# Kernel optimization log

Measured on AMD Instinct MI355X. Metric: run time of the kernel, lower is better.

The kernel has to match this reference:

```python
import jax, jax.numpy as jnp
import numpy as np

# Dims
B, L = 64, 64            # bs*n_vars, patch_num
C, K = 32, 100           # cluster_num, top-k tokens per cluster
D_MODEL, H, D_LLM = 128, 8, 768
D_KEYS = D_MODEL // H    # 16
TEMP = 1.0 / np.sqrt(D_KEYS)
SCALE = 0.02             # param init scale for numerical stability


def setup_inputs() -> dict:
    key = jax.random.key(0)
    ks = jax.random.split(key, 8)
    return {
        "topk_token_embeddings": jax.random.normal(ks[0], (C, K, D_LLM), jnp.float32),
        "ts_emb": jax.random.normal(ks[1], (B, L, D_MODEL), jnp.float32),
        "cluster_probs": jax.random.uniform(ks[2], (B, L, C), jnp.float32),
        # per-cluster projections; last input column is a fused bias (+1 dim)
        "Wq": jax.random.normal(ks[3], (C, H * D_KEYS, D_MODEL + 1), jnp.float32) * SCALE,
        "Wk": jax.random.normal(ks[4], (C, H * D_KEYS, D_LLM + 1), jnp.float32) * SCALE,
        "Wv": jax.random.normal(ks[5], (C, H * D_KEYS, D_LLM + 1), jnp.float32) * SCALE,
        "Wo": jax.random.normal(ks[6], (C, H, D_KEYS, D_LLM), jnp.float32) * SCALE,
        "bo": jax.random.normal(ks[7], (C, D_LLM), jnp.float32) * SCALE,
    }


def reference(topk_token_embeddings, ts_emb, cluster_probs, Wq, Wk, Wv, Wo, bo):
    # Per-cluster Q projection: (B,L,C,H*dk) -> (B,L,C,H,dk)
    q = jnp.einsum('bld,cgd->blcg', ts_emb, Wq[..., :-1]) + Wq[..., -1]
    q = q.reshape(B, L, C, H, D_KEYS)
    # Per-cluster K/V projections: (K,C,H*dk) -> (K,C,H,dk)
    k = jnp.einsum('ckd,cgd->kcg', topk_token_embeddings, Wk[..., :-1]) + Wk[..., -1]
    k = k.reshape(K, C, H, D_KEYS)
    v = jnp.einsum('ckd,cgd->kcg', topk_token_embeddings, Wv[..., :-1]) + Wv[..., -1]
    v = v.reshape(K, C, H, D_KEYS)
    # Attention over token axis k with extra cluster axis c
    att = jnp.einsum('blchd,kchd->bchlk', q, k)          # (B,C,H,L,K)
    att = jax.nn.softmax(TEMP * att, axis=-1)            # dropout is identity in eval
    out = jnp.einsum('bchlk,kchd->bclhd', att, v)        # (B,C,L,H,dk)
    # Per-cluster output projection to d_llm
    aligned = jnp.einsum('bclhd,chde->blce', out, Wo) + bo  # (B,L,C,d_llm)
    # TSAligner: cluster-probability weighted sum over clusters
    fused = jnp.sum(aligned * cluster_probs[:, :, :, None], axis=-2)  # (B,L,d_llm)
    return fused
```

## Files before the change

kernel.cpp:

```cpp
#include <hip/hip_runtime.h>
#include <stdint.h>

#define NB 64
#define NL 64
#define NC 32
#define NK 100
#define NH 8
#define DKEY 16
#define DM 128
#define NG 128
#define DLLM 768
#define KP 4128
#define TEMP 0.25f
#define QSCL 0.3606737602222409f

typedef __attribute__((ext_vector_type(8))) short bf16x8;
typedef __attribute__((ext_vector_type(4))) short bf16x4;
typedef __attribute__((ext_vector_type(4))) float f32x4;

typedef uint32_t __attribute__((address_space(1))) gu32;
typedef uint32_t __attribute__((address_space(3))) lu32;

__device__ __forceinline__ void gload_lds16(const void* g, void* l) {
    __builtin_amdgcn_global_load_lds((const gu32*)g, (lu32*)l, 16, 0, 0);
}

__device__ __forceinline__ uint16_t f2bf(float f) {
    union { float f; uint32_t i; } x; x.f = f;
    uint32_t r = x.i + 0x7FFFu + ((x.i >> 16) & 1u);
    return (uint16_t)(r >> 16);
}
__device__ __forceinline__ uint32_t pack2(float lo, float hi) {
    return (uint32_t)f2bf(lo) | ((uint32_t)f2bf(hi) << 16);
}
__device__ __forceinline__ uint32_t cvtpk_bf16(float lo, float hi) {
    uint32_t r;
    asm("v_cvt_pk_bf16_f32 %0, %1, %2" : "=v"(r) : "v"(lo), "v"(hi));
    return r;
}

__global__ __launch_bounds__(256) void convert_in_kernel(
    const float* __restrict__ ts,
    const float* __restrict__ Wq,
    uint16_t* __restrict__ tsbf,
    uint16_t* __restrict__ wqbf)
{
    int i = blockIdx.x * 256 + threadIdx.x;
    if (i < 524288) {
        tsbf[i] = f2bf(ts[i]);
    } else {
        int j = i - 524288;
        wqbf[j] = f2bf(Wq[(j >> 7) * 129 + (j & 127)]);
    }
}

__global__ __launch_bounds__(256) void convert_kv_kernel(
    const float* __restrict__ topk,
    const float* __restrict__ Wk,
    const float* __restrict__ Wv,
    uint16_t* __restrict__ topkbf,
    uint16_t* __restrict__ wkbf,
    uint16_t* __restrict__ wvbf)
{
    int r = blockIdx.x;
    int t = threadIdx.x;
    if (r < 3200) {
        if (t < 192) {
            float4 v = *(const float4*)(topk + (size_t)r * 768 + t * 4);
            uint2 u;
            u.x = pack2(v.x, v.y);
            u.y = pack2(v.z, v.w);
            *(uint2*)(topkbf + (size_t)r * 768 + t * 4) = u;
        }
    } else {
        int rr = r - 3200;
        const float* src;
        uint16_t* dst;
        if (rr < 4096) {
            src = Wk + (size_t)rr * 769;
            dst = wkbf + (size_t)rr * 768;
        } else {
            rr -= 4096;
            src = Wv + (size_t)rr * 769;
            dst = wvbf + (size_t)rr * 768;
        }
#pragma unroll
        for (int i = 0; i < 3; ++i)
            dst[t + 256 * i] = f2bf(src[t + 256 * i]);
    }
}

__global__ __launch_bounds__(256) void kv_mfma_kernel(
    const uint16_t* __restrict__ topkbf,
    const uint16_t* __restrict__ wkbf,
    const uint16_t* __restrict__ wvbf,
    const float* __restrict__ Wk,
    const float* __restrict__ Wv,
    uint16_t* __restrict__ kbuf,
    uint16_t* __restrict__ vbufT)
{
    __shared__ short As[2][2048];
    __shared__ short Bs[2][2048];

    int bid = blockIdx.x;
    int nb = bid & 1;
    int mb = (bid >> 1) & 1;
    int c  = (bid >> 2) & 31;
    int which = bid >> 7;

    int tid  = threadIdx.x;
    int lane = tid & 63;
    int w    = tid >> 6;
    int wr   = w >> 1;
    int wc   = w & 1;
    int r16  = lane & 15;
    int kp   = lane >> 4;

    int arow = mb * 64 + w * 16 + r16;
    int brow = nb * 64 + w * 16 + r16;
    const uint16_t* aptr;
    const uint16_t* bptr;
    if (which == 0) {
        aptr = topkbf + ((size_t)(c * 100 + arow)) * 768 + kp * 8;
        bptr = wkbf   + ((size_t)(c * 128 + brow)) * 768 + kp * 8;
    } else {
        aptr = wvbf   + ((size_t)(c * 128 + arow)) * 768 + kp * 8;
        bptr = topkbf + ((size_t)(c * 100 + brow)) * 768 + kp * 8;
    }

    short* adst[2] = { &As[0][w * 512], &As[1][w * 512] };
    short* bdst[2] = { &Bs[0][w * 512], &Bs[1][w * 512] };

    f32x4 acc[2][2] = {};

    gload_lds16(aptr, adst[0]);
    gload_lds16(bptr, bdst[0]);
    __syncthreads();

    int cur = 0;
    for (int kt = 0; kt < 24; ++kt) {
        if (kt < 23) {
            gload_lds16(aptr + (kt + 1) * 32, adst[cur ^ 1]);
            gload_lds16(bptr + (kt + 1) * 32, bdst[cur ^ 1]);
        }
        const short* Ab = As[cur];
        const short* Bb = Bs[cur];
        bf16x8 a0 = *(const bf16x8*)(Ab + (wr * 2 + 0) * 512 + lane * 8);
        bf16x8 a1 = *(const bf16x8*)(Ab + (wr * 2 + 1) * 512 + lane * 8);
        bf16x8 b0 = *(const bf16x8*)(Bb + (wc * 2 + 0) * 512 + lane * 8);
        bf16x8 b1 = *(const bf16x8*)(Bb + (wc * 2 + 1) * 512 + lane * 8);
        acc[0][0] = __builtin_amdgcn_mfma_f32_16x16x32_bf16(a0, b0, acc[0][0], 0, 0, 0);
        acc[0][1] = __builtin_amdgcn_mfma_f32_16x16x32_bf16(a0, b1, acc[0][1], 0, 0, 0);
        acc[1][0] = __builtin_amdgcn_mfma_f32_16x16x32_bf16(a1, b0, acc[1][0], 0, 0, 0);
        acc[1][1] = __builtin_amdgcn_mfma_f32_16x16x32_bf16(a1, b1, acc[1][1], 0, 0, 0);
        __syncthreads();
        cur ^= 1;
    }

    int mbase = mb * 64 + wr * 32 + (lane >> 4) * 4;
    int nbase = nb * 64 + wc * 32 + (lane & 15);

    if (which == 0) {
        float bias0 = Wk[((size_t)c * 128 + nbase)      * 769 + 768];
        float bias1 = Wk[((size_t)c * 128 + nbase + 16) * 769 + 768];
#pragma unroll
        for (int fm = 0; fm < 2; ++fm)
#pragma unroll
            for (int r = 0; r < 4; ++r) {
                int mrow = mbase + fm * 16 + r;
                if (mrow < 112) {
                    kbuf[((size_t)c * 112 + mrow) * 128 + nbase]      = f2bf(acc[fm][0][r] + bias0);
                    kbuf[((size_t)c * 112 + mrow) * 128 + nbase + 16] = f2bf(acc[fm][1][r] + bias1);
                }
            }
    } else {
#pragma unroll
        for (int fm = 0; fm < 2; ++fm)
#pragma unroll
            for (int r = 0; r < 4; ++r) {
                int grow = mbase + fm * 16 + r;
                float bias = Wv[((size_t)c * 128 + grow) * 769 + 768];
#pragma unroll
                for (int fn = 0; fn < 2; ++fn) {
                    int ncol = nbase + fn * 16;
                    uint16_t val = (ncol < NK) ? f2bf(acc[fm][fn][r] + bias) : (uint16_t)0;
                    vbufT[((size_t)c * 128 + grow) * 128 + ncol] = val;
                }
            }
    }
}

__global__ __launch_bounds__(256) void q_proj_mfma_kernel(
    const uint16_t* __restrict__ tsbf,
    const uint16_t* __restrict__ wqbf,
    const float* __restrict__ Wq,
    uint16_t* __restrict__ qbuf)
{
    __shared__ short As[2][4096];
    __shared__ short Bs[2][4096];

    int bid = blockIdx.x;
    int mb = bid & 31;
    int c  = bid >> 5;

    int tid  = threadIdx.x;
    int lane = tid & 63;
    int w    = tid >> 6;
    int wr   = w >> 1;
    int wc   = w & 1;

    int sg  = tid >> 6;
    int skp = (tid >> 4) & 3;
    int sr  = tid & 15;
    const uint16_t* aptr = tsbf + ((size_t)(mb * 128 + sg * 16 + sr)) * 128 + skp * 8;
    const uint16_t* bptr = wqbf + ((size_t)(c * 128 + sg * 16 + sr)) * 128 + skp * 8;

    short* adst[2] = { &As[0][w * 512], &As[1][w * 512] };
    short* bdst[2] = { &Bs[0][w * 512], &Bs[1][w * 512] };

    f32x4 acc[4][4] = {};

    gload_lds16(aptr, adst[0]);
    gload_lds16(aptr + (size_t)64 * 128, adst[0] + 2048);
    gload_lds16(bptr, bdst[0]);
    gload_lds16(bptr + (size_t)64 * 128, bdst[0] + 2048);
    __syncthreads();

    int cur = 0;
    for (int kt = 0; kt < 4; ++kt) {
        if (kt < 3) {
            const uint16_t* ap = aptr + (kt + 1) * 32;
            const uint16_t* bp = bptr + (kt + 1) * 32;
            gload_lds16(ap, adst[cur ^ 1]);
            gload_lds16(ap + (size_t)64 * 128, adst[cur ^ 1] + 2048);
            gload_lds16(bp, bdst[cur ^ 1]);
            gload_lds16(bp + (size_t)64 * 128, bdst[cur ^ 1] + 2048);
        }
        const short* Ab = As[cur];
        const short* Bb = Bs[cur];
        bf16x8 av[4], bv[4];
#pragma unroll
        for (int m = 0; m < 4; ++m)
            av[m] = *(const bf16x8*)(Ab + (wr * 4 + m) * 512 + lane * 8);
#pragma unroll
        for (int n = 0; n < 4; ++n)
            bv[n] = *(const bf16x8*)(Bb + (wc * 4 + n) * 512 + lane * 8);
#pragma unroll
        for (int m = 0; m < 4; ++m)
#pragma unroll
            for (int n = 0; n < 4; ++n)
                acc[m][n] = __builtin_amdgcn_mfma_f32_16x16x32_bf16(av[m], bv[n], acc[m][n], 0, 0, 0);
        __syncthreads();
        cur ^= 1;
    }

    int mbase = mb * 128 + wr * 64 + (lane >> 4) * 4;
    int nfix  = wc * 64 + (lane & 15);
#pragma unroll
    for (int n = 0; n < 4; ++n) {
        int ncol = nfix + n * 16;
        float bias = Wq[((size_t)c * 128 + ncol) * 129 + 128];
#pragma unroll
        for (int m = 0; m < 4; ++m)
#pragma unroll
            for (int r = 0; r < 4; ++r)
                qbuf[((size_t)c * 4096 + mbase + m * 16 + r) * 128 + ncol] =
                    f2bf((acc[m][n][r] + bias) * QSCL);
    }
}

__global__ __launch_bounds__(256) void attn_mfma_kernel(
    const uint16_t* __restrict__ qbuf,
    const uint16_t* __restrict__ kbuf,
    const uint16_t* __restrict__ vbufT,
    const float* __restrict__ probs,
    uint16_t* __restrict__ wout)
{
    __shared__ short Pl[4][64][128];

    int bid = blockIdx.x;
    int c = bid >> 6;
    int b = bid & 63;
    int tid = threadIdx.x;
    int lane = tid & 63;
    int w = tid >> 6;
    int g = lane >> 4;
    int l15 = lane & 15;
    int swz = l15 << 4;

    float pr_tok = probs[((size_t)b * 64 + lane) * NC + c];

    uint8_t* Pb = (uint8_t*)&Pl[w][0][0];
    bf16x8 zf = {};
    const short ob = (short)0x3F80;
    bf16x8 ones = { ob, ob, ob, ob, ob, ob, ob, ob };

    for (int hh = 0; hh < 2; ++hh) {
        int h = w * 2 + hh;

        bf16x8 qb[4];
#pragma unroll
        for (int nt = 0; nt < 4; ++nt) {
            if (g < 2)
                qb[nt] = *(const bf16x8*)&qbuf[((size_t)c * 4096 + b * 64 + nt * 16 + l15) * 128 + h * 16 + g * 8];
            else
                qb[nt] = zf;
        }

#pragma unroll
        for (int mt = 0; mt < 7; ++mt) {
            bf16x8 ka;
            if (g < 2)
                ka = *(const bf16x8*)&kbuf[((size_t)c * 112 + mt * 16 + l15) * 128 + h * 16 + g * 8];
            else
                ka = zf;
            f32x4 s[4];
#pragma unroll
            for (int nt = 0; nt < 4; ++nt)
                s[nt] = __builtin_amdgcn_mfma_f32_16x16x32_bf16(ka, qb[nt], (f32x4){0.f,0.f,0.f,0.f}, 0, 0, 0);
            bool valid = (mt < 6) || (g == 0);
#pragma unroll
            for (int nt = 0; nt < 4; ++nt) {
                float p0 = valid ? __builtin_exp2f(s[nt][0]) : 0.f;
                float p1 = valid ? __builtin_exp2f(s[nt][1]) : 0.f;
                float p2 = valid ? __builtin_exp2f(s[nt][2]) : 0.f;
                float p3 = valid ? __builtin_exp2f(s[nt][3]) : 0.f;
                union { uint32_t u[2]; bf16x4 v; } pk;
                pk.u[0] = cvtpk_bf16(p0, p1);
                pk.u[1] = cvtpk_bf16(p2, p3);
                int l = nt * 16 + l15;
                *(bf16x4*)(Pb + l * 256 + ((mt * 32 + g * 8) ^ swz)) = pk.v;
            }
        }
        {
            bf16x4 z4 = {};
#pragma unroll
            for (int nt = 0; nt < 4; ++nt) {
                int l = nt * 16 + l15;
                *(bf16x4*)(Pb + l * 256 + ((224 + g * 8) ^ swz)) = z4;
            }
        }
        asm volatile("s_waitcnt lgkmcnt(0)" ::: "memory");

        f32x4 oacc[4] = {};
        f32x4 osum[4] = {};
#pragma unroll
        for (int ch = 0; ch < 4; ++ch) {
            bf16x8 vb = *(const bf16x8*)&vbufT[((size_t)c * 128 + h * 16 + l15) * 128 + ch * 32 + g * 8];
#pragma unroll
            for (int mt = 0; mt < 4; ++mt) {
                int l = mt * 16 + l15;
                bf16x8 pa = *(const bf16x8*)(Pb + l * 256 + ((ch * 64 + g * 16) ^ swz));
                oacc[mt] = __builtin_amdgcn_mfma_f32_16x16x32_bf16(pa, vb, oacc[mt], 0, 0, 0);
                osum[mt] = __builtin_amdgcn_mfma_f32_16x16x32_bf16(pa, ones, osum[mt], 0, 0, 0);
            }
        }
#pragma unroll
        for (int mt = 0; mt < 4; ++mt) {
#pragma unroll
            for (int r = 0; r < 4; ++r) {
                int l = mt * 16 + g * 4 + r;
                float sc = __shfl(pr_tok, l) * __builtin_amdgcn_rcpf(osum[mt][r]);
                wout[((size_t)b * 64 + l) * KP + c * 128 + h * 16 + l15] =
                    f2bf(oacc[mt][r] * sc);
            }
        }
        asm volatile("s_waitcnt lgkmcnt(0)" ::: "memory");
    }
    if (tid < 64)
        wout[((size_t)b * 64 + tid) * KP + 4096 + c] = f2bf(pr_tok);
}

__global__ __launch_bounds__(256) void convert_wo_kernel(
    const float* __restrict__ Wo,
    const float* __restrict__ bo,
    uint16_t* __restrict__ wobt)
{
    __shared__ float tile[32][65];
    int bid = blockIdx.x;
    int kt = bid / 12;
    int nb = bid % 12;
    int t = threadIdx.x;
    {
        int rr = t >> 3;
        int c0 = (t & 7) * 8;
        int kg = kt * 32 + rr;
        const float* src = (kg < 4096 ? Wo + (size_t)kg * DLLM
                                      : bo + (size_t)(kg - 4096) * DLLM)
                           + nb * 64 + c0;
        float4 v0 = *(const float4*)src;
        float4 v1 = *(const float4*)(src + 4);
        tile[rr][c0 + 0] = v0.x; tile[rr][c0 + 1] = v0.y;
        tile[rr][c0 + 2] = v0.z; tile[rr][c0 + 3] = v0.w;
        tile[rr][c0 + 4] = v1.x; tile[rr][c0 + 5] = v1.y;
        tile[rr][c0 + 6] = v1.z; tile[rr][c0 + 7] = v1.w;
    }
    __syncthreads();
    {
        int n  = t >> 2;
        int k0 = (t & 3) * 8;
        uint4 u;
        u.x = pack2(tile[k0 + 0][n], tile[k0 + 1][n]);
        u.y = pack2(tile[k0 + 2][n], tile[k0 + 3][n]);
        u.z = pack2(tile[k0 + 4][n], tile[k0 + 5][n]);
        u.w = pack2(tile[k0 + 6][n], tile[k0 + 7][n]);
        *(uint4*)&wobt[((size_t)(nb * 64 + n)) * KP + kt * 32 + k0] = u;
    }
}

__global__ __launch_bounds__(256) void fgemm_splitk_kernel(
    const uint16_t* __restrict__ wout,
    const uint16_t* __restrict__ wobt,
    float* __restrict__ part)
{
    __shared__ short As[2][4096];
    __shared__ short Bs[2][4096];

    int bid = blockIdx.x;
    int swz = (bid & 7) * 48 + (bid >> 3);
    int h  = swz / 192;
    int rr = swz - h * 192;
    int mb = rr / 6;
    int nb = rr - mb * 6;

    int tid  = threadIdx.x;
    int lane = tid & 63;
    int w    = tid >> 6;
    int wr   = w >> 1;
    int wc   = w & 1;

    int sg = tid >> 6;
    int skp = (tid >> 4) & 3;
    int sr = tid & 15;
    const uint16_t* aptr = wout + ((size_t)(mb * 128 + sg * 16 + sr)) * KP + h * 2048 + skp * 8;
    const uint16_t* bptr = wobt + ((size_t)(nb * 128 + sg * 16 + sr)) * KP + h * 2048 + skp * 8;

    short* adst[2] = { &As[0][w * 512], &As[1][w * 512] };
    short* bdst[2] = { &Bs[0][w * 512], &Bs[1][w * 512] };

    int nkt = h ? 65 : 64;

    f32x4 acc[4][4] = {};

    gload_lds16(aptr, adst[0]);
    gload_lds16(aptr + (size_t)64 * KP, adst[0] + 2048);
    gload_lds16(bptr, bdst[0]);
    gload_lds16(bptr + (size_t)64 * KP, bdst[0] + 2048);
    __syncthreads();

    int cur = 0;
    for (int kt = 0; kt < nkt; ++kt) {
        if (kt + 1 < nkt) {
            const uint16_t* ap = aptr + (size_t)(kt + 1) * 32;
            const uint16_t* bp = bptr + (size_t)(kt + 1) * 32;
            gload_lds16(ap, adst[cur ^ 1]);
            gload_lds16(ap + (size_t)64 * KP, adst[cur ^ 1] + 2048);
            gload_lds16(bp, bdst[cur ^ 1]);
            gload_lds16(bp + (size_t)64 * KP, bdst[cur ^ 1] + 2048);
        }
        const short* Ab = As[cur];
        const short* Bb = Bs[cur];
        bf16x8 av[4], bv[4];
#pragma unroll
        for (int m = 0; m < 4; ++m)
            av[m] = *(const bf16x8*)(Ab + (wr * 4 + m) * 512 + lane * 8);
#pragma unroll
        for (int n = 0; n < 4; ++n)
            bv[n] = *(const bf16x8*)(Bb + (wc * 4 + n) * 512 + lane * 8);
#pragma unroll
        for (int m = 0; m < 4; ++m)
#pragma unroll
            for (int n = 0; n < 4; ++n)
                acc[m][n] = __builtin_amdgcn_mfma_f32_16x16x32_bf16(av[m], bv[n], acc[m][n], 0, 0, 0);
        __syncthreads();
        cur ^= 1;
    }

    float* P = part + (size_t)h * (4096 * 768);
    int mbase = mb * 128 + wr * 64 + (lane >> 4) * 4;
    int nbase = nb * 128 + wc * 64 + (lane & 15);
#pragma unroll
    for (int m = 0; m < 4; ++m)
#pragma unroll
        for (int n = 0; n < 4; ++n)
#pragma unroll
            for (int r = 0; r < 4; ++r)
                P[(size_t)(mbase + m * 16 + r) * DLLM + nbase + n * 16] =
                    acc[m][n][r];
}

__global__ __launch_bounds__(256) void reduce_out_kernel(
    const float* __restrict__ part,
    float* __restrict__ out)
{
    int i = (blockIdx.x * 256 + threadIdx.x) * 4;
    float4 a = *(const float4*)(part + i);
    float4 b = *(const float4*)(part + 4096 * 768 + i);
    float4 s;
    s.x = a.x + b.x; s.y = a.y + b.y; s.z = a.z + b.z; s.w = a.w + b.w;
    *(float4*)(out + i) = s;
}

extern "C" void kernel_launch(void* const* d_in, const int* in_sizes, int n_in,
                              void* d_out, int out_size, void* d_ws, size_t ws_size,
                              hipStream_t stream) {
    const float* topk  = (const float*)d_in[0];
    const float* ts    = (const float*)d_in[1];
    const float* probs = (const float*)d_in[2];
    const float* Wq    = (const float*)d_in[3];
    const float* Wk    = (const float*)d_in[4];
    const float* Wv    = (const float*)d_in[5];
    const float* Wo    = (const float*)d_in[6];
    const float* bo    = (const float*)d_in[7];
    float* out = (float*)d_out;

    uint16_t* ws    = (uint16_t*)d_ws;
    uint16_t* kbuf  = ws;
    uint16_t* vbufT = ws + 458752;
    uint16_t* qbuf  = ws + 983040;
    uint16_t* wout  = ws + 983040 + 16777216;
    uint16_t* tsbf   = wout;
    uint16_t* wqbf   = wout + 524288;
    uint16_t* topkbf = wout + 1048576;
    uint16_t* wkbf   = wout + 1048576 + 2457600;
    uint16_t* wvbf   = wout + 1048576 + 2457600 + 3145728;
    uint16_t* wobt = qbuf;
    float*    part = (float*)(qbuf + 3170304);

    convert_in_kernel<<<4096, 256, 0, stream>>>(ts, Wq, tsbf, wqbf);
    convert_kv_kernel<<<11392, 256, 0, stream>>>(topk, Wk, Wv, topkbf, wkbf, wvbf);
    kv_mfma_kernel<<<256, 256, 0, stream>>>(topkbf, wkbf, wvbf, Wk, Wv, kbuf, vbufT);
    q_proj_mfma_kernel<<<1024, 256, 0, stream>>>(tsbf, wqbf, Wq, qbuf);
    attn_mfma_kernel<<<2048, 256, 0, stream>>>(qbuf, kbuf, vbufT, probs, wout);
    convert_wo_kernel<<<1548, 256, 0, stream>>>(Wo, bo, wobt);
    fgemm_splitk_kernel<<<384, 256, 0, stream>>>(wout, wobt, part);
    reduce_out_kernel<<<3072, 256, 0, stream>>>(part, out);
}
```

Measured before the change: 172.4 us.

## Merge conversion kernels and compute softmax row sums in registers

```diff
diff --git a/kernel.cpp b/kernel.cpp
--- a/kernel.cpp
+++ b/kernel.cpp
@@ -39,54 +39,88 @@
     return r;
 }
 
-__global__ __launch_bounds__(256) void convert_in_kernel(
+__global__ __launch_bounds__(256) void convert_all_kernel(
     const float* __restrict__ ts,
     const float* __restrict__ Wq,
-    uint16_t* __restrict__ tsbf,
-    uint16_t* __restrict__ wqbf)
-{
-    int i = blockIdx.x * 256 + threadIdx.x;
-    if (i < 524288) {
-        tsbf[i] = f2bf(ts[i]);
-    } else {
-        int j = i - 524288;
-        wqbf[j] = f2bf(Wq[(j >> 7) * 129 + (j & 127)]);
-    }
-}
-
-__global__ __launch_bounds__(256) void convert_kv_kernel(
     const float* __restrict__ topk,
     const float* __restrict__ Wk,
     const float* __restrict__ Wv,
+    const float* __restrict__ Wo,
+    const float* __restrict__ bo,
+    uint16_t* __restrict__ tsbf,
+    uint16_t* __restrict__ wqbf,
     uint16_t* __restrict__ topkbf,
     uint16_t* __restrict__ wkbf,
-    uint16_t* __restrict__ wvbf)
-{
-    int r = blockIdx.x;
+    uint16_t* __restrict__ wvbf,
+    uint16_t* __restrict__ wobt)
+{
+    __shared__ float tile[32][65];
+    int bid = blockIdx.x;
     int t = threadIdx.x;
-    if (r < 3200) {
-        if (t < 192) {
-            float4 v = *(const float4*)(topk + (size_t)r * 768 + t * 4);
-            uint2 u;
-            u.x = pack2(v.x, v.y);
-            u.y = pack2(v.z, v.w);
-            *(uint2*)(topkbf + (size_t)r * 768 + t * 4) = u;
+
+    if (bid < 4096) {
+        int i = bid * 256 + t;
+        if (i < 524288) {
+            tsbf[i] = f2bf(ts[i]);
+        } else {
+            int j = i - 524288;
+            wqbf[j] = f2bf(Wq[(j >> 7) * 129 + (j & 127)]);
+        }
+    } else if (bid < 15488) {
+        int r = bid - 4096;
+        if (r < 3200) {
+            if (t < 192) {
+                float4 v = *(const float4*)(topk + (size_t)r * 768 + t * 4);
+                uint2 u;
+                u.x = pack2(v.x, v.y);
+                u.y = pack2(v.z, v.w);
+                *(uint2*)(topkbf + (size_t)r * 768 + t * 4) = u;
+            }
+        } else {
+            int rr = r - 3200;
+            const float* src;
+            uint16_t* dst;
+            if (rr < 4096) {
+                src = Wk + (size_t)rr * 769;
+                dst = wkbf + (size_t)rr * 768;
+            } else {
+                rr -= 4096;
+                src = Wv + (size_t)rr * 769;
+                dst = wvbf + (size_t)rr * 768;
+            }
+#pragma unroll
+            for (int i = 0; i < 3; ++i)
+                dst[t + 256 * i] = f2bf(src[t + 256 * i]);
         }
     } else {
-        int rr = r - 3200;
-        const float* src;
-        uint16_t* dst;
-        if (rr < 4096) {
-            src = Wk + (size_t)rr * 769;
-            dst = wkbf + (size_t)rr * 768;
-        } else {
-            rr -= 4096;
-            src = Wv + (size_t)rr * 769;
-            dst = wvbf + (size_t)rr * 768;
-        }
-#pragma unroll
-        for (int i = 0; i < 3; ++i)
-            dst[t + 256 * i] = f2bf(src[t + 256 * i]);
+        int b2 = bid - 15488;
+        int kt = b2 / 12;
+        int nb = b2 % 12;
+        {
+            int rr = t >> 3;
+            int c0 = (t & 7) * 8;
+            int kg = kt * 32 + rr;
+            const float* src = (kg < 4096 ? Wo + (size_t)kg * DLLM
+                                          : bo + (size_t)(kg - 4096) * DLLM)
+                               + nb * 64 + c0;
+            float4 v0 = *(const float4*)src;
+            float4 v1 = *(const float4*)(src + 4);
+            tile[rr][c0 + 0] = v0.x; tile[rr][c0 + 1] = v0.y;
+            tile[rr][c0 + 2] = v0.z; tile[rr][c0 + 3] = v0.w;
+            tile[rr][c0 + 4] = v1.x; tile[rr][c0 + 5] = v1.y;
+            tile[rr][c0 + 6] = v1.z; tile[rr][c0 + 7] = v1.w;
+        }
+        __syncthreads();
+        {
+            int n  = t >> 2;
+            int k0 = (t & 3) * 8;
+            uint4 u;
+            u.x = pack2(tile[k0 + 0][n], tile[k0 + 1][n]);
+            u.y = pack2(tile[k0 + 2][n], tile[k0 + 3][n]);
+            u.z = pack2(tile[k0 + 4][n], tile[k0 + 5][n]);
+            u.w = pack2(tile[k0 + 6][n], tile[k0 + 7][n]);
+            *(uint4*)&wobt[((size_t)(nb * 64 + n)) * KP + kt * 32 + k0] = u;
+        }
     }
 }
 
@@ -292,8 +326,6 @@
 
     uint8_t* Pb = (uint8_t*)&Pl[w][0][0];
     bf16x8 zf = {};
-    const short ob = (short)0x3F80;
-    bf16x8 ones = { ob, ob, ob, ob, ob, ob, ob, ob };
 
     for (int hh = 0; hh < 2; ++hh) {
         int h = w * 2 + hh;
@@ -307,6 +339,7 @@
                 qb[nt] = zf;
         }
 
+        float psum[4] = {0.f, 0.f, 0.f, 0.f};
 #pragma unroll
         for (int mt = 0; mt < 7; ++mt) {
             bf16x8 ka;
@@ -325,6 +358,7 @@
                 float p1 = valid ? __builtin_exp2f(s[nt][1]) : 0.f;
                 float p2 = valid ? __builtin_exp2f(s[nt][2]) : 0.f;
                 float p3 = valid ? __builtin_exp2f(s[nt][3]) : 0.f;
+                psum[nt] += (p0 + p1) + (p2 + p3);
                 union { uint32_t u[2]; bf16x4 v; } pk;
                 pk.u[0] = cvtpk_bf16(p0, p1);
                 pk.u[1] = cvtpk_bf16(p2, p3);
@@ -340,10 +374,18 @@
                 *(bf16x4*)(Pb + l * 256 + ((224 + g * 8) ^ swz)) = z4;
             }
         }
-        asm volatile("s_waitcnt lgkmcnt(0)" ::: "memory");
+        __syncthreads();
+
+        float rsum[4];
+#pragma unroll
+        for (int nt = 0; nt < 4; ++nt) {
+            float t = psum[nt];
+            t += __shfl_xor(t, 16);
+            t += __shfl_xor(t, 32);
+            rsum[nt] = __builtin_amdgcn_rcpf(t);
+        }
 
         f32x4 oacc[4] = {};
-        f32x4 osum[4] = {};
 #pragma unroll
         for (int ch = 0; ch < 4; ++ch) {
             bf16x8 vb = *(const bf16x8*)&vbufT[((size_t)c * 128 + h * 16 + l15) * 128 + ch * 32 + g * 8];
@@ -352,7 +394,6 @@
                 int l = mt * 16 + l15;
                 bf16x8 pa = *(const bf16x8*)(Pb + l * 256 + ((ch * 64 + g * 16) ^ swz));
                 oacc[mt] = __builtin_amdgcn_mfma_f32_16x16x32_bf16(pa, vb, oacc[mt], 0, 0, 0);
-                osum[mt] = __builtin_amdgcn_mfma_f32_16x16x32_bf16(pa, ones, osum[mt], 0, 0, 0);
             }
         }
 #pragma unroll
@@ -360,12 +401,12 @@
 #pragma unroll
             for (int r = 0; r < 4; ++r) {
                 int l = mt * 16 + g * 4 + r;
-                float sc = __shfl(pr_tok, l) * __builtin_amdgcn_rcpf(osum[mt][r]);
+                float sc = __shfl(pr_tok, l) * __shfl(rsum[mt], g * 4 + r);
                 wout[((size_t)b * 64 + l) * KP + c * 128 + h * 16 + l15] =
                     f2bf(oacc[mt][r] * sc);
             }
         }
-        asm volatile("s_waitcnt lgkmcnt(0)" ::: "memory");
+        __syncthreads();
     }
     if (tid < 64)
         wout[((size_t)b * 64 + tid) * KP + 4096 + c] = f2bf(pr_tok);
@@ -524,15 +565,20 @@
     uint16_t* topkbf = wout + 1048576;
     uint16_t* wkbf   = wout + 1048576 + 2457600;
     uint16_t* wvbf   = wout + 1048576 + 2457600 + 3145728;
-    uint16_t* wobt = qbuf;
-    float*    part = (float*)(qbuf + 3170304);
-
-    convert_in_kernel<<<4096, 256, 0, stream>>>(ts, Wq, tsbf, wqbf);
-    convert_kv_kernel<<<11392, 256, 0, stream>>>(topk, Wk, Wv, topkbf, wkbf, wvbf);
+    float* part = (float*)(qbuf + 3170304);
+
+    const size_t BASE = 34668544;
+    bool slack = ws_size >= (BASE + 3170304) * sizeof(uint16_t);
+    uint16_t* wobt = slack ? (ws + BASE) : qbuf;
+
+    int nconv = slack ? 17036 : 15488;
+    convert_all_kernel<<<nconv, 256, 0, stream>>>(ts, Wq, topk, Wk, Wv, Wo, bo,
+                                                  tsbf, wqbf, topkbf, wkbf, wvbf, wobt);
     kv_mfma_kernel<<<256, 256, 0, stream>>>(topkbf, wkbf, wvbf, Wk, Wv, kbuf, vbufT);
     q_proj_mfma_kernel<<<1024, 256, 0, stream>>>(tsbf, wqbf, Wq, qbuf);
     attn_mfma_kernel<<<2048, 256, 0, stream>>>(qbuf, kbuf, vbufT, probs, wout);
-    convert_wo_kernel<<<1548, 256, 0, stream>>>(Wo, bo, wobt);
+    if (!slack)
+        convert_wo_kernel<<<1548, 256, 0, stream>>>(Wo, bo, wobt);
     fgemm_splitk_kernel<<<384, 256, 0, stream>>>(wout, wobt, part);
     reduce_out_kernel<<<3072, 256, 0, stream>>>(part, out);
 }
```

Measured after the change: 168.3 us. 2.4% less time.
